# Optimization experiments

Hardware: AMD Instinct MI355X
Metric: run time of the kernel (lower is better)

## Reference

```python
import jax, jax.numpy as jnp
import numpy as np

NUM_ENT = 100000
NUM_REL = 500            # distinct relations; table holds 2*NUM_REL (forward + inverse)
E = 500000               # total edges: first half original, second half reversed
D = 200                  # init_dim = gcn_dim = embed_dim
B = 256
KW, KH = 10, 20          # ConvE reshape: 2*KW*KH == 2*D
NF, KS = 200, 7
FLAT = (2 * KW - KS + 1) * (KH - KS + 1) * NF  # 14*14*200 = 39200
EPS = 1e-5


def setup_inputs() -> dict:
    key = jax.random.key(0)
    k = jax.random.split(key, 24)
    half = E // 2
    src = jax.random.randint(k[0], (half,), 0, NUM_ENT)
    dst = jax.random.randint(k[1], (half,), 0, NUM_ENT)
    et = jax.random.randint(k[2], (half,), 0, NUM_REL)
    edge_index = jnp.stack([jnp.concatenate([src, dst]), jnp.concatenate([dst, src])])
    edge_type = jnp.concatenate([et, et + NUM_REL])
    sub = jax.random.randint(k[3], (B,), 0, NUM_ENT)
    rel = jax.random.randint(k[4], (B,), 0, 2 * NUM_REL)
    g = lambda i, shape, s=0.05: jax.random.normal(k[i], shape, jnp.float32) * s
    return dict(
        sub=sub, rel=rel, edge_index=edge_index, edge_type=edge_type,
        init_embed=g(5, (NUM_ENT, D)), init_rel=g(6, (2 * NUM_REL, D)),
        loop_rel1=g(7, (1, D)), loop_rel2=g(8, (1, D)),
        w_in1=g(9, (D, D)), w_out1=g(10, (D, D)), w_loop1=g(11, (D, D)), w_rel1=g(12, (D, D)), b1=jnp.zeros((D,), jnp.float32),
        w_in2=g(13, (D, D)), w_out2=g(14, (D, D)), w_loop2=g(15, (D, D)), w_rel2=g(16, (D, D)), b2=jnp.zeros((D,), jnp.float32),
        conv_w=g(17, (NF, 1, KS, KS)), conv_b=jnp.zeros((NF,), jnp.float32),
        bn0_g=jnp.ones((1,), jnp.float32), bn0_b=jnp.zeros((1,), jnp.float32),
        bn1_g=jnp.ones((NF,), jnp.float32), bn1_b=jnp.zeros((NF,), jnp.float32),
        bn2_g=jnp.ones((D,), jnp.float32), bn2_b=jnp.zeros((D,), jnp.float32),
        fc_w=g(18, (FLAT, D)), fc_b=jnp.zeros((D,), jnp.float32),
        ent_bias=jnp.zeros((NUM_ENT,), jnp.float32),
    )


def _bn2d(x, g, b):  # eval-mode BN: running mean 0, running var 1
    s = g / jnp.sqrt(1.0 + EPS)
    return x * s[None, :, None, None] + b[None, :, None, None]


def _bn1d(x, g, b):
    return x * (g / jnp.sqrt(1.0 + EPS)) + b


def _agg(x_src, rel_e, dst, w):
    # message = comp(h_src, h_rel) @ W   (subtraction composition), degree-normalized scatter
    m = (x_src - rel_e) @ w                                        # [E/2, D]
    s = jax.ops.segment_sum(m, dst, num_segments=NUM_ENT)          # [N, D]
    deg = jax.ops.segment_sum(jnp.ones(dst.shape, m.dtype), dst, num_segments=NUM_ENT)
    return s / jnp.clip(deg, 1.0)[:, None]


def _ragcn_layer(x, r, ei, et, w_in, w_out, w_loop, w_rel, loop_rel, b):
    half = ei.shape[1] // 2
    src, dst = ei[0], ei[1]
    re = r[et]                                                     # [E, D]
    res = (_agg(x[src[:half]], re[:half], dst[:half], w_in)
           + _agg(x[src[half:]], re[half:], dst[half:], w_out)
           + (x - loop_rel) @ w_loop)
    return jnp.tanh(res / 3.0 + b), r @ w_rel


def _forward(sub, rel, edge_index, edge_type, init_embed, init_rel,
             loop_rel1, loop_rel2, w_in1, w_out1, w_loop1, w_rel1, b1,
             w_in2, w_out2, w_loop2, w_rel2, b2, conv_w, conv_b,
             bn0_g, bn0_b, bn1_g, bn1_b, bn2_g, bn2_b, fc_w, fc_b, ent_bias):
    x, r = _ragcn_layer(init_embed, init_rel, edge_index, edge_type, w_in1, w_out1, w_loop1, w_rel1, loop_rel1, b1)
    x, r = _ragcn_layer(x, r, edge_index, edge_type, w_in2, w_out2, w_loop2, w_rel2, loop_rel2, b2)
    sub_emb = x[sub]                                               # [B, D]
    rel_emb = r[rel]                                               # [B, D]
    # ConvE concat: [B,2,D] -> [B,D,2] -> [B,1,2*KW,KH]
    stk = jnp.transpose(jnp.stack([sub_emb, rel_emb], axis=1), (0, 2, 1)).reshape(-1, 1, 2 * KW, KH)
    h = _bn2d(stk, bn0_g, bn0_b)
    h = jax.lax.conv_general_dilated(h, conv_w, (1, 1), 'VALID',
                                     dimension_numbers=('NCHW', 'OIHW', 'NCHW'))
    h = h + conv_b[None, :, None, None]
    h = jax.nn.relu(_bn2d(h, bn1_g, bn1_b))
    h = h.reshape(-1, FLAT)
    h = h @ fc_w + fc_b
    h = jax.nn.relu(_bn1d(h, bn2_g, bn2_b))
    logits = h @ x.T + ent_bias                                    # [B, NUM_ENT]
    return jax.nn.sigmoid(logits)


def reference(sub, rel, edge_index, edge_type, init_embed, init_rel,
              loop_rel1, loop_rel2, w_in1, w_out1, w_loop1, w_rel1, b1,
              w_in2, w_out2, w_loop2, w_rel2, b2, conv_w, conv_b,
              bn0_g, bn0_b, bn1_g, bn1_b, bn2_g, bn2_b, fc_w, fc_b, ent_bias):
    return _forward(sub, rel, edge_index, edge_type, init_embed, init_rel,
                    loop_rel1, loop_rel2, w_in1, w_out1, w_loop1, w_rel1, b1,
                    w_in2, w_out2, w_loop2, w_rel2, b2, conv_w, conv_b,
                    bn0_g, bn0_b, bn1_g, bn1_b, bn2_g, bn2_b, fc_w, fc_b, ent_bias)
```

## Files before the change

### kernel.cpp

```cpp
#include <hip/hip_runtime.h>
#include <math.h>

#define N_ENT   100000
#define N_REL2  1000
#define E_TOT   500000
#define E_HALF  250000
#define DIM     200
#define BB      256
#define NFILT   200
#define FLATK   39200
#define EPS_BN  1e-5f

#define NROWS   200000
#define SCHUNK  2048
#define SNBLK   ((NROWS + SCHUNK - 1) / SCHUNK)

#define FC_KC   175
#define FC_KLEN 224

typedef __attribute__((ext_vector_type(8))) short bf16x8;
typedef __attribute__((ext_vector_type(4))) float f32x4;

__device__ __forceinline__ unsigned short f2b(float f) {
    union { float f; unsigned u; } c; c.f = f;
    unsigned u = c.u;
    u += 0x7fffu + ((u >> 16) & 1u);
    return (unsigned short)(u >> 16);
}
__device__ __forceinline__ float b2f(unsigned short h) {
    union { unsigned u; float f; } c; c.u = ((unsigned)h) << 16;
    return c.f;
}
__device__ __forceinline__ float fast_tanh(float x) {
    float ax = fabsf(x);
    float e = __expf(-2.0f * ax);
    float t = (1.0f - e) / (1.0f + e);
    return copysignf(t, x);
}

__global__ void convert2_kernel(const float* __restrict__ s1, unsigned short* __restrict__ d1,
                                int n1, const float* __restrict__ s2,
                                unsigned short* __restrict__ d2, int n2, int nb1) {
    int b = blockIdx.x;
    const float* s; unsigned short* d; int n, base;
    if (b < nb1) { s = s1; d = d1; n = n1; base = b; }
    else         { s = s2; d = d2; n = n2; base = b - nb1; }
    int i = (base * 256 + threadIdx.x) * 4;
    if (i + 3 < n) {
        float4 v = *(const float4*)(s + i);
        ushort4 o;
        o.x = f2b(v.x); o.y = f2b(v.y); o.z = f2b(v.z); o.w = f2b(v.w);
        *(ushort4*)(d + i) = o;
    } else {
        for (; i < n; ++i) d[i] = f2b(s[i]);
    }
}

__global__ void wstack_lv_kernel(const float* __restrict__ wIn, const float* __restrict__ wOut,
                                 const float* __restrict__ wLoop,
                                 const float* __restrict__ lr, float* __restrict__ lv,
                                 unsigned short* __restrict__ WTK) {
    if (blockIdx.x == 588) {
        int j = threadIdx.x;
        if (j < DIM) {
            float acc = 0.f;
            for (int k = 0; k < DIM; ++k) acc += lr[k] * wLoop[k * DIM + j];
            lv[j] = acc;
        }
        return;
    }
    int g = blockIdx.x * 256 + threadIdx.x;
    int kk = g & 7;
    int t = g >> 3;
    int col = t % 224;
    int t2 = t / 224;
    int unit = t2 % 28;
    int seg = t2 / 28;
    int k = unit * 8 + kk;
    float v = 0.f;
    if (col < 200 && k < 200)
        v = (seg == 0 ? wIn : seg == 1 ? wOut : wLoop)[k * 200 + col];
    WTK[g] = f2b(v);
}

__global__ void fwt_cwt_kernel(const float* __restrict__ fw, unsigned short* __restrict__ FWT,
                               const float* __restrict__ cw, unsigned short* __restrict__ CWT) {
    __shared__ float t[32][33];
    const int bid = blockIdx.x;
    const int tid = threadIdx.x;
    if (bid >= 8575) {
        int g = (bid - 8575) * 256 + tid;
        int f = g >> 6, k = g & 63;
        CWT[g] = (f < 200 && k < 49) ? f2b(cw[f * 49 + k]) : 0;
        return;
    }
    const int kt = bid % 1225, jt = bid / 1225;
#pragma unroll
    for (int it = 0; it < 4; ++it) {
        int idx = tid + it * 256;
        int kk = idx >> 5, jj = idx & 31;
        int j = jt * 32 + jj;
        t[kk][jj] = (j < 200) ? fw[(size_t)(kt * 32 + kk) * 200 + j] : 0.f;
    }
    __syncthreads();
#pragma unroll
    for (int it = 0; it < 4; ++it) {
        int idx = tid + it * 256;
        int jj = idx >> 5, kk = idx & 31;
        int j = jt * 32 + jj;
        if (j < 208)
            FWT[(size_t)j * FLATK + kt * 32 + kk] = f2b(t[kk][jj]);
    }
}

__global__ void hist_kernel(const int* __restrict__ ei, int* __restrict__ cnt) {
    int e = blockIdx.x * 256 + threadIdx.x;
    if (e >= E_TOT) return;
    int row = ei[E_TOT + e] + (e < E_HALF ? 0 : N_ENT);
    atomicAdd(&cnt[row], 1);
}

__global__ void scan1_kernel(const int* __restrict__ cnt, int* __restrict__ row_start,
                             int* __restrict__ blockSum) {
    __shared__ int tsum[256];
    const int t = threadIdx.x;
    const int base = blockIdx.x * SCHUNK + t * 8;
    int v[8];
    int s = 0;
#pragma unroll
    for (int i = 0; i < 8; ++i) {
        int idx = base + i;
        int c = (idx < NROWS) ? cnt[idx] : 0;
        v[i] = s;
        s += c;
    }
    tsum[t] = s;
    __syncthreads();
    for (int off = 1; off < 256; off <<= 1) {
        int x = (t >= off) ? tsum[t - off] : 0;
        __syncthreads();
        if (t >= off) tsum[t] += x;
        __syncthreads();
    }
    int texc = (t == 0) ? 0 : tsum[t - 1];
    if (t == 0) blockSum[blockIdx.x] = tsum[255];
#pragma unroll
    for (int i = 0; i < 8; ++i) {
        int idx = base + i;
        if (idx < NROWS) row_start[idx] = texc + v[i];
    }
}

__global__ void scan2_kernel(int* __restrict__ blockSum) {
    __shared__ int t[128];
    int i = threadIdx.x;
    int v = (i < SNBLK) ? blockSum[i] : 0;
    t[i] = v;
    __syncthreads();
    for (int off = 1; off < 128; off <<= 1) {
        int x = (i >= off) ? t[i - off] : 0;
        __syncthreads();
        t[i] += x;
        __syncthreads();
    }
    if (i < SNBLK) blockSum[i] = (i == 0) ? 0 : t[i - 1];
}

__global__ void scan3_kernel(int* __restrict__ row_start, int* __restrict__ row_cur,
                             const int* __restrict__ blockSum) {
    int i = blockIdx.x * 256 + threadIdx.x;
    if (i >= NROWS) return;
    int v = row_start[i] + blockSum[i / SCHUNK];
    row_start[i] = v;
    row_cur[i] = v;
}

__global__ void fill_kernel(const int* __restrict__ ei, const int* __restrict__ et,
                            int* __restrict__ row_cur, int2* __restrict__ epair) {
    int e = blockIdx.x * 256 + threadIdx.x;
    if (e >= E_TOT) return;
    int row = ei[E_TOT + e] + (e < E_HALF ? 0 : N_ENT);
    int pos = atomicAdd(&row_cur[row], 1);
    epair[pos] = make_int2(ei[e], et[e]);
}

__global__ void gather_kernel(const unsigned short* __restrict__ x,
                              const unsigned short* __restrict__ r,
                              const int2* __restrict__ epair,
                              const int* __restrict__ row_start, const int* __restrict__ cnt,
                              unsigned short* __restrict__ agg) {
    int wid = blockIdx.x * 4 + (threadIdx.x >> 6);
    if (wid >= NROWS) return;
    int lane = threadIdx.x & 63;
    if (lane >= 50) return;
    int start = row_start[wid];
    int deg = cnt[wid];
    float a0 = 0.f, a1 = 0.f, a2 = 0.f, a3 = 0.f;
    float c0 = 0.f, c1 = 0.f, c2 = 0.f, c3 = 0.f;
    int i = 0;
    for (; i + 2 <= deg; i += 2) {
        int2 e0 = epair[start + i];
        int2 e1 = epair[start + i + 1];
        ushort4 xv0 = *(const ushort4*)(x + (size_t)e0.x * DIM + lane * 4);
        ushort4 rv0 = *(const ushort4*)(r + (size_t)e0.y * DIM + lane * 4);
        ushort4 xv1 = *(const ushort4*)(x + (size_t)e1.x * DIM + lane * 4);
        ushort4 rv1 = *(const ushort4*)(r + (size_t)e1.y * DIM + lane * 4);
        a0 += b2f(xv0.x) - b2f(rv0.x);
        a1 += b2f(xv0.y) - b2f(rv0.y);
        a2 += b2f(xv0.z) - b2f(rv0.z);
        a3 += b2f(xv0.w) - b2f(rv0.w);
        c0 += b2f(xv1.x) - b2f(rv1.x);
        c1 += b2f(xv1.y) - b2f(rv1.y);
        c2 += b2f(xv1.z) - b2f(rv1.z);
        c3 += b2f(xv1.w) - b2f(rv1.w);
    }
    if (i < deg) {
        int2 e = epair[start + i];
        ushort4 xv = *(const ushort4*)(x + (size_t)e.x * DIM + lane * 4);
        ushort4 rv = *(const ushort4*)(r + (size_t)e.y * DIM + lane * 4);
        a0 += b2f(xv.x) - b2f(rv.x);
        a1 += b2f(xv.y) - b2f(rv.y);
        a2 += b2f(xv.z) - b2f(rv.z);
        a3 += b2f(xv.w) - b2f(rv.w);
    }
    float sc = 1.0f / fmaxf((float)deg, 1.0f);
    ushort4 o;
    o.x = f2b((a0 + c0) * sc);
    o.y = f2b((a1 + c1) * sc);
    o.z = f2b((a2 + c2) * sc);
    o.w = f2b((a3 + c3) * sc);
    *(ushort4*)(agg + (size_t)wid * DIM + lane * 4) = o;
}

__global__ void rgemm_kernel(const float* __restrict__ r, const float* __restrict__ w,
                             float* __restrict__ out, unsigned short* __restrict__ outb,
                             int rows) {
    int g = blockIdx.x * 256 + threadIdx.x;
    if (g >= rows * DIM) return;
    int i = g / DIM, j = g - i * DIM;
    float acc = 0.f;
    for (int k = 0; k < DIM; ++k) acc += r[i * DIM + k] * w[k * DIM + j];
    out[g] = acc;
    if (outb) outb[g] = f2b(acc);
}

#define LOAD_A1(g, slot) do {                                                   \
    const unsigned short* Ap_ = Aseg[(g) / 7];                                  \
    apf[slot] = *(const bf16x8*)(Ap_ + (size_t)arow * 200 + ((g) % 7) * 32 + lq * 8); \
} while (0)

#define STAGE_LOAD(s) do {                                                       \
    _Pragma("unroll")                                                            \
    for (int it = 0; it < 4; ++it) {                                             \
        int u = tid + it * 256;                                                  \
        if (u < 896) {                                                           \
            int slot = u / 448;                                                  \
            int rem  = u - slot * 448;                                           \
            int ui   = rem / 112, col = rem - ui * 112;                          \
            int g2   = (s) * 2 + slot;                                           \
            if (g2 < 21) {                                                       \
                int sg = g2 / 7, kc = g2 % 7;                                    \
                vals[it] = *(const int4*)(WTK +                                  \
                    ((size_t)(sg * 28 + kc * 4 + ui) * 224 + colbase + col) * 8);\
            } else vals[it] = make_int4(0, 0, 0, 0);                             \
        }                                                                        \
    }                                                                            \
} while (0)

#define STAGE_WRITE(b) do {                                                      \
    _Pragma("unroll")                                                            \
    for (int it = 0; it < 4; ++it) {                                             \
        int u = tid + it * 256;                                                  \
        if (u < 896) *(int4*)(&Wl[(b)][u * 8]) = vals[it];                       \
    }                                                                            \
} while (0)

__global__ __launch_bounds__(256, 4) void layer_mfma_kernel(
        const unsigned short* __restrict__ aggI, const unsigned short* __restrict__ aggO,
        const unsigned short* __restrict__ xin, const unsigned short* __restrict__ WTK,
        const float* __restrict__ lv, const float* __restrict__ bias,
        unsigned short* __restrict__ out, int nwg) {
    __shared__ unsigned short Wl[2][8 * 112 * 8];
    const int bid = blockIdx.x;
    const int q = nwg >> 3, rr = nwg & 7;
    const int xcd = bid & 7, idx = bid >> 3;
    const int L = (xcd < rr ? xcd * (q + 1) : rr * (q + 1) + (xcd - rr) * q) + idx;
    const int rowblk  = L >> 1;
    const int colbase = (L & 1) * 112;

    const int tid  = threadIdx.x;
    const int wm   = tid >> 6;
    const int lane = tid & 63;
    const int lr   = lane & 15;
    const int lq   = lane >> 4;
    const int row0 = rowblk * 64;
    const int arow = row0 + wm * 16 + lr;

    const unsigned short* const Aseg[3] = { aggI, aggO, xin };

    f32x4 acc[7];
#pragma unroll
    for (int n = 0; n < 7; ++n) acc[n] = (f32x4){0.f, 0.f, 0.f, 0.f};

    bf16x8 apf[4];
    LOAD_A1(0, 0);
    LOAD_A1(1, 1);
    LOAD_A1(2, 2);

    int4 vals[4];

    STAGE_LOAD(0);
    STAGE_WRITE(0);
    __syncthreads();

#pragma unroll
    for (int p = 0; p < 11; ++p) {
        if (p < 10) STAGE_LOAD(p + 1);
        const int NC = (p < 10) ? 2 : 1;
#pragma unroll
        for (int cc = 0; cc < NC; ++cc) {
            const int g = p * 2 + cc;
            if (g + 3 < 21) LOAD_A1(g + 3, (g + 3) & 3);
            __builtin_amdgcn_s_setprio(1);
#pragma unroll
            for (int n = 0; n < 7; ++n) {
                bf16x8 b = *(const bf16x8*)(&Wl[p & 1][((cc * 4 + lq) * 112 + n * 16 + lr) * 8]);
                acc[n] = __builtin_amdgcn_mfma_f32_16x16x32_bf16(apf[g & 3], b, acc[n], 0, 0, 0);
            }
            __builtin_amdgcn_s_setprio(0);
        }
        if (p < 10) STAGE_WRITE((p + 1) & 1);
        __syncthreads();
    }

    {
        int rbase = row0 + wm * 16 + lq * 4;
#pragma unroll
        for (int n = 0; n < 7; ++n) {
            int col = colbase + n * 16 + lr;
            if (col < 200) {
                float lvc = lv[col], bc = bias[col];
#pragma unroll
                for (int r2 = 0; r2 < 4; ++r2) {
                    int row = rbase + r2;
                    if (row < N_ENT) {
                        float v = (acc[n][r2] - lvc) * (1.0f / 3.0f) + bc;
                        out[(size_t)row * 200 + col] = f2b(fast_tanh(v));
                    }
                }
            }
        }
    }
}

__global__ void img_kernel(const unsigned short* __restrict__ x, const float* __restrict__ r,
                           const int* __restrict__ sub, const int* __restrict__ rel,
                           const float* __restrict__ bn0g, const float* __restrict__ bn0b,
                           unsigned short* __restrict__ img) {
    int g = blockIdx.x * 256 + threadIdx.x;
    if (g >= BB * 2 * DIM) return;
    int b = g / 400, l = g - b * 400;
    int d = l >> 1;
    float v = (l & 1) ? r[(size_t)rel[b] * DIM + d] : b2f(x[(size_t)sub[b] * DIM + d]);
    float s0 = bn0g[0] * rsqrtf(1.0f + EPS_BN);
    img[g] = f2b(v * s0 + bn0b[0]);
}

__global__ void im2col_kernel(const unsigned short* __restrict__ img,
                              unsigned short* __restrict__ IM) {
    int g = blockIdx.x * 256 + threadIdx.x;
    if (g >= 50176 * 64) return;
    int row = g >> 6, k = g & 63;
    int b = row / 196, p = row - b * 196;
    int h = p / 14, w = p - h * 14;
    unsigned short v = 0;
    if (k < 49) {
        int i = k / 7, j = k - i * 7;
        v = img[b * 400 + (h + i) * 20 + (w + j)];
    }
    IM[g] = v;
}

__global__ __launch_bounds__(256) void conv_mfma_kernel(
        const unsigned short* __restrict__ IM, const unsigned short* __restrict__ CWT,
        const float* __restrict__ cb, const float* __restrict__ bn1g,
        const float* __restrict__ bn1b, unsigned short* __restrict__ CO_B) {
    const int tid  = threadIdx.x;
    const int row0 = blockIdx.x * 128;
    const int wave = tid >> 6;
    const int lane = tid & 63;
    const int lr   = lane & 15;
    const int lq   = lane >> 4;
    const int arow = row0 + wave * 32 + lr;

    f32x4 acc[2][13];
#pragma unroll
    for (int m = 0; m < 2; ++m)
#pragma unroll
        for (int n = 0; n < 13; ++n) acc[m][n] = (f32x4){0.f, 0.f, 0.f, 0.f};

#pragma unroll
    for (int c = 0; c < 2; ++c) {
        const int k = c * 32 + lq * 8;
        bf16x8 a0 = *(const bf16x8*)(IM + (size_t)arow * 64 + k);
        bf16x8 a1 = *(const bf16x8*)(IM + (size_t)(arow + 16) * 64 + k);
#pragma unroll
        for (int n = 0; n < 13; ++n) {
            bf16x8 b = *(const bf16x8*)(CWT + (size_t)(n * 16 + lr) * 64 + k);
            acc[0][n] = __builtin_amdgcn_mfma_f32_16x16x32_bf16(a0, b, acc[0][n], 0, 0, 0);
            acc[1][n] = __builtin_amdgcn_mfma_f32_16x16x32_bf16(a1, b, acc[1][n], 0, 0, 0);
        }
    }

#pragma unroll
    for (int m = 0; m < 2; ++m) {
        int grow_base = row0 + wave * 32 + m * 16 + lq * 4;
#pragma unroll
        for (int n = 0; n < 13; ++n) {
            int col = n * 16 + lr;
            if (col < 200) {
                float s1 = bn1g[col] * rsqrtf(1.0f + EPS_BN);
                float t1 = bn1b[col];
                float cbf = cb[col];
#pragma unroll
                for (int r = 0; r < 4; ++r) {
                    int grow = grow_base + r;
                    int b = grow / 196, p = grow - b * 196;
                    float v = fmaxf((acc[m][n][r] + cbf) * s1 + t1, 0.f);
                    CO_B[(size_t)b * FLATK + col * 196 + p] = f2b(v);
                }
            }
        }
    }
}

__global__ __launch_bounds__(256) void fc_mfma_kernel(
        const unsigned short* __restrict__ CO_B, const unsigned short* __restrict__ FWT,
        float* __restrict__ partials) {
    const int tid  = threadIdx.x;
    const int kc   = blockIdx.x >> 2;
    const int mb   = blockIdx.x & 3;
    const int wave = tid >> 6;
    const int lane = tid & 63;
    const int lr   = lane & 15;
    const int lq   = lane >> 4;
    const int m0   = mb * 64 + wave * 16;

    f32x4 acc[13];
#pragma unroll
    for (int n = 0; n < 13; ++n) acc[n] = (f32x4){0.f, 0.f, 0.f, 0.f};

#pragma unroll
    for (int s = 0; s < 7; ++s) {
        const int k = kc * FC_KLEN + s * 32 + lq * 8;
        bf16x8 a = *(const bf16x8*)(CO_B + (size_t)(m0 + lr) * FLATK + k);
#pragma unroll
        for (int n = 0; n < 13; ++n) {
            bf16x8 b = *(const bf16x8*)(FWT + (size_t)(n * 16 + lr) * FLATK + k);
            acc[n] = __builtin_amdgcn_mfma_f32_16x16x32_bf16(a, b, acc[n], 0, 0, 0);
        }
    }

    float* slab = partials + (size_t)kc * (BB * 208);
#pragma unroll
    for (int n = 0; n < 13; ++n) {
        int col = n * 16 + lr;
#pragma unroll
        for (int r = 0; r < 4; ++r) {
            int row = m0 + lq * 4 + r;
            slab[(size_t)row * 208 + col] = acc[n][r];
        }
    }
}

__global__ void fc_reduce_kernel(const float* __restrict__ partials,
                                 const float* __restrict__ fcb,
                                 const float* __restrict__ g2, const float* __restrict__ b2v,
                                 unsigned short* __restrict__ hb) {
    int g = blockIdx.x * 256 + threadIdx.x;
    if (g >= BB * 224) return;
    int b = g / 224, j = g - b * 224;
    unsigned short o = 0;
    if (j < 200) {
        float s = 0.f;
        const float* p = partials + (size_t)b * 208 + j;
#pragma unroll 5
        for (int c = 0; c < FC_KC; ++c)
            s += p[(size_t)c * (BB * 208)];
        float v = (s + fcb[j]) * (g2[j] * rsqrtf(1.0f + EPS_BN)) + b2v[j];
        o = f2b(fmaxf(v, 0.f));
    }
    hb[g] = o;
}

#define LOAD_HB(g, buf) do {                                                    \
    const unsigned short* base_ = hb + (size_t)brow * 224 + (g) * 32 + lq * 8;  \
    buf[0] = *(const bf16x8*)(base_);                                           \
    buf[1] = *(const bf16x8*)(base_ + 16 * 224);                                \
} while (0)

__global__ __launch_bounds__(512, 2) void logits_mfma_kernel(
        const unsigned short* __restrict__ x, const unsigned short* __restrict__ hb,
        const float* __restrict__ eb, float* __restrict__ out, int nwg) {
    __shared__ unsigned short Xl[112 * 136];
    const int bid = blockIdx.x;
    const int q = nwg >> 3, rr = nwg & 7;
    const int xcd = bid & 7, idx = bid >> 3;
    const int nb = (xcd < rr ? xcd * (q + 1) : rr * (q + 1) + (xcd - rr) * q) + idx;
    const int ent0 = nb * 112;

    const int tid  = threadIdx.x;
    const int wave = tid >> 6;
    const int mh   = wave >> 2;
    const int wm   = wave & 3;
    const int lane = tid & 63;
    const int lr   = lane & 15;
    const int lq   = lane >> 4;
    const int brow = mh * 128 + wm * 32 + lr;

    f32x4 acc[2][7];
#pragma unroll
    for (int m = 0; m < 2; ++m)
#pragma unroll
        for (int n = 0; n < 7; ++n) acc[m][n] = (f32x4){0.f, 0.f, 0.f, 0.f};

    bf16x8 apf[3][2];
    LOAD_HB(0, apf[0]);
    LOAD_HB(1, apf[1]);

#pragma unroll
    for (int ph = 0; ph < 2; ++ph) {
        if (ph) __syncthreads();
        if (ph == 0) {
#pragma unroll
            for (int it = 0; it < 4; ++it) {
                int u = tid + it * 512;
                if (u < 1792) {
                    int row = u >> 4, c = u & 15;
                    int ent = ent0 + row;
                    int4 v = make_int4(0, 0, 0, 0);
                    if (ent < N_ENT)
                        v = *(const int4*)(x + (size_t)ent * 200 + c * 8);
                    *(int4*)(&Xl[row * 136 + c * 8]) = v;
                }
            }
        } else {
            for (int u = tid; u < 1344; u += 512) {
                int row = u / 12, c = u - row * 12;
                int gu = 16 + c;
                int ent = ent0 + row;
                int4 v = make_int4(0, 0, 0, 0);
                if (ent < N_ENT && gu < 25)
                    v = *(const int4*)(x + (size_t)ent * 200 + gu * 8);
                *(int4*)(&Xl[row * 136 + c * 8]) = v;
            }
        }
        __syncthreads();
        const int NC = (ph == 0) ? 4 : 3;
#pragma unroll
        for (int cc = 0; cc < NC; ++cc) {
            const int g = (ph ? 4 : 0) + cc;
            if (g + 2 < 7) LOAD_HB(g + 2, apf[(g + 2) % 3]);
#pragma unroll
            for (int n = 0; n < 7; ++n) {
                bf16x8 b = *(const bf16x8*)(&Xl[(n * 16 + lr) * 136 + cc * 32 + lq * 8]);
                acc[0][n] = __builtin_amdgcn_mfma_f32_16x16x32_bf16(apf[g % 3][0], b, acc[0][n], 0, 0, 0);
                acc[1][n] = __builtin_amdgcn_mfma_f32_16x16x32_bf16(apf[g % 3][1], b, acc[1][n], 0, 0, 0);
            }
        }
    }

#pragma unroll
    for (int m = 0; m < 2; ++m) {
        int b_base = mh * 128 + wm * 32 + m * 16 + lq * 4;
#pragma unroll
        for (int n = 0; n < 7; ++n) {
            int ent = ent0 + n * 16 + lr;
            if (ent < N_ENT) {
                float bias = eb[ent];
#pragma unroll
                for (int r = 0; r < 4; ++r) {
                    float v = acc[m][n][r] + bias;
                    out[(size_t)(b_base + r) * N_ENT + ent] = 1.0f / (1.0f + __expf(-v));
                }
            }
        }
    }
}

extern "C" void kernel_launch(void* const* d_in, const int* in_sizes, int n_in,
                              void* d_out, int out_size, void* d_ws, size_t ws_size,
                              hipStream_t stream) {
    const int*   sub        = (const int*)  d_in[0];
    const int*   rel        = (const int*)  d_in[1];
    const int*   edge_index = (const int*)  d_in[2];
    const int*   edge_type  = (const int*)  d_in[3];
    const float* init_embed = (const float*)d_in[4];
    const float* init_rel   = (const float*)d_in[5];
    const float* loop_rel1  = (const float*)d_in[6];
    const float* loop_rel2  = (const float*)d_in[7];
    const float* w_in1      = (const float*)d_in[8];
    const float* w_out1     = (const float*)d_in[9];
    const float* w_loop1    = (const float*)d_in[10];
    const float* w_rel1     = (const float*)d_in[11];
    const float* b1         = (const float*)d_in[12];
    const float* w_in2      = (const float*)d_in[13];
    const float* w_out2     = (const float*)d_in[14];
    const float* w_loop2    = (const float*)d_in[15];
    const float* w_rel2     = (const float*)d_in[16];
    const float* b2         = (const float*)d_in[17];
    const float* conv_w     = (const float*)d_in[18];
    const float* conv_b     = (const float*)d_in[19];
    const float* bn0_g      = (const float*)d_in[20];
    const float* bn0_b      = (const float*)d_in[21];
    const float* bn1_g      = (const float*)d_in[22];
    const float* bn1_b      = (const float*)d_in[23];
    const float* bn2_g      = (const float*)d_in[24];
    const float* bn2_b      = (const float*)d_in[25];
    const float* fc_w       = (const float*)d_in[26];
    const float* fc_b       = (const float*)d_in[27];
    const float* ent_bias   = (const float*)d_in[28];

    unsigned short* aggb = (unsigned short*)d_ws;
    unsigned short* x0b  = aggb + 40000000;
    unsigned short* x1b  = x0b  + 20000000;
    unsigned short* r0b  = x1b  + 20000000;
    unsigned short* r1b  = r0b  + 200000;
    unsigned short* WTK  = r1b  + 200000;
    unsigned short* img  = WTK  + 150528;
    unsigned short* IM   = img  + 102400;
    unsigned short* CWT  = IM   + 3211264;
    unsigned short* CO_B = CWT  + 13312;
    unsigned short* hb16 = CO_B + 10035200;
    unsigned short* FWT  = hb16 + 57344;
    float* fbase = (float*)(FWT + 8153600);
    float* r1f      = fbase;
    float* r2f      = r1f  + 200000;
    float* lv       = r2f  + 200000;
    float* partials = lv   + 256;

    int2* epair    = (int2*)CO_B;
    int* cnt       = (int*)(epair + E_TOT);
    int* row_start = cnt  + NROWS;
    int* row_cur   = row_start + NROWS;
    int* blockSum  = row_cur + NROWS;

    unsigned short* aggIb = aggb;
    unsigned short* aggOb = aggb + (size_t)N_ENT * DIM;
    unsigned short* x2b   = x0b;

    const int gather_blocks = (NROWS + 3) / 4;
    const int layer_nwg     = ((N_ENT + 63) / 64) * 2;
    const int logits_nwg    = (N_ENT + 111) / 112;
    const int cvt_nb1       = (N_ENT * DIM / 4 + 255) / 256;
    const int cvt_nb2       = (N_REL2 * DIM / 4 + 255) / 256;

    convert2_kernel<<<cvt_nb1 + cvt_nb2, 256, 0, stream>>>(init_embed, x0b, N_ENT * DIM,
                                                           init_rel, r0b, N_REL2 * DIM, cvt_nb1);
    hipMemsetAsync(cnt, 0, (size_t)NROWS * 4, stream);
    hist_kernel<<<(E_TOT + 255) / 256, 256, 0, stream>>>(edge_index, cnt);
    scan1_kernel<<<SNBLK, 256, 0, stream>>>(cnt, row_start, blockSum);
    scan2_kernel<<<1, 128, 0, stream>>>(blockSum);
    scan3_kernel<<<(NROWS + 255) / 256, 256, 0, stream>>>(row_start, row_cur, blockSum);
    fill_kernel<<<(E_TOT + 255) / 256, 256, 0, stream>>>(edge_index, edge_type, row_cur, epair);

    wstack_lv_kernel<<<589, 256, 0, stream>>>(w_in1, w_out1, w_loop1, loop_rel1, lv, WTK);
    gather_kernel<<<gather_blocks, 256, 0, stream>>>(x0b, r0b, epair, row_start, cnt, aggb);
    layer_mfma_kernel<<<layer_nwg, 256, 0, stream>>>(aggIb, aggOb, x0b, WTK, lv, b1, x1b, layer_nwg);
    rgemm_kernel<<<(N_REL2 * DIM + 255) / 256, 256, 0, stream>>>(init_rel, w_rel1, r1f, r1b, N_REL2);

    wstack_lv_kernel<<<589, 256, 0, stream>>>(w_in2, w_out2, w_loop2, loop_rel2, lv, WTK);
    gather_kernel<<<gather_blocks, 256, 0, stream>>>(x1b, r1b, epair, row_start, cnt, aggb);
    layer_mfma_kernel<<<layer_nwg, 256, 0, stream>>>(aggIb, aggOb, x1b, WTK, lv, b2, x2b, layer_nwg);
    rgemm_kernel<<<(N_REL2 * DIM + 255) / 256, 256, 0, stream>>>(r1f, w_rel2, r2f,
                                                                 (unsigned short*)nullptr, N_REL2);

    img_kernel<<<(BB * 400 + 255) / 256, 256, 0, stream>>>(x2b, r2f, sub, rel,
                                                           bn0_g, bn0_b, img);
    im2col_kernel<<<(50176 * 64 + 255) / 256, 256, 0, stream>>>(img, IM);
    fwt_cwt_kernel<<<8575 + 52, 256, 0, stream>>>(fc_w, FWT, conv_w, CWT);
    conv_mfma_kernel<<<50176 / 128, 256, 0, stream>>>(IM, CWT, conv_b, bn1_g, bn1_b, CO_B);
    fc_mfma_kernel<<<FC_KC * 4, 256, 0, stream>>>(CO_B, FWT, partials);
    fc_reduce_kernel<<<(BB * 224 + 255) / 256, 256, 0, stream>>>(partials, fc_b, bn2_g, bn2_b, hb16);

    logits_mfma_kernel<<<logits_nwg, 512, 0, stream>>>(x2b, hb16, ent_bias, (float*)d_out,
                                                       logits_nwg);
}
```

Measured before the change: 557.3 us.

## Stream layer weights directly into LDS and fuse image build into im2col

The layer GEMM now stages weight tiles with direct global-to-LDS loads instead of going through registers and then a separate LDS write. This frees registers and drops the extra write step. Separately, the img kernel is merged into im2col, so each im2col element reads the embeddings directly and applies the BN0 scaling, which removes one launch and one intermediate buffer. The direct LDS loads rely on the asynchronous load being ordered before the existing barrier, and the fused im2col repeats the gather and scaling for each of the 49 taps.

```diff
diff --git a/kernel.cpp b/kernel.cpp
--- a/kernel.cpp
+++ b/kernel.cpp
@@ -20,6 +20,9 @@
 
 typedef __attribute__((ext_vector_type(8))) short bf16x8;
 typedef __attribute__((ext_vector_type(4))) float f32x4;
+
+#define GLOBAL_AS __attribute__((address_space(1)))
+#define LDS_AS    __attribute__((address_space(3)))
 
 __device__ __forceinline__ unsigned short f2b(float f) {
     union { float f; unsigned u; } c; c.f = f;
@@ -249,29 +252,22 @@
     apf[slot] = *(const bf16x8*)(Ap_ + (size_t)arow * 200 + ((g) % 7) * 32 + lq * 8); \
 } while (0)
 
-#define STAGE_LOAD(s) do {                                                       \
+#define STAGE_GLD(s, b) do {                                                     \
     _Pragma("unroll")                                                            \
     for (int it = 0; it < 4; ++it) {                                             \
         int u = tid + it * 256;                                                  \
-        if (u < 896) {                                                           \
-            int slot = u / 448;                                                  \
-            int rem  = u - slot * 448;                                           \
-            int ui   = rem / 112, col = rem - ui * 112;                          \
-            int g2   = (s) * 2 + slot;                                           \
-            if (g2 < 21) {                                                       \
-                int sg = g2 / 7, kc = g2 % 7;                                    \
-                vals[it] = *(const int4*)(WTK +                                  \
-                    ((size_t)(sg * 28 + kc * 4 + ui) * 224 + colbase + col) * 8);\
-            } else vals[it] = make_int4(0, 0, 0, 0);                             \
+        int slot = u / 448;                                                      \
+        int rem  = u - slot * 448;                                               \
+        int ui   = rem / 112, col = rem - ui * 112;                              \
+        int g2   = (s) * 2 + slot;                                               \
+        if (u < 896 && g2 < 21) {                                                \
+            int sg = g2 / 7, kc = g2 % 7;                                        \
+            const unsigned short* gp = WTK +                                     \
+                ((size_t)(sg * 28 + kc * 4 + ui) * 224 + colbase + col) * 8;     \
+            __builtin_amdgcn_global_load_lds(                                    \
+                (const GLOBAL_AS unsigned int*)(const void*)gp,                  \
+                (LDS_AS unsigned int*)(void*)(&Wl[(b)][u * 8]), 16, 0, 0);       \
         }                                                                        \
-    }                                                                            \
-} while (0)
-
-#define STAGE_WRITE(b) do {                                                      \
-    _Pragma("unroll")                                                            \
-    for (int it = 0; it < 4; ++it) {                                             \
-        int u = tid + it * 256;                                                  \
-        if (u < 896) *(int4*)(&Wl[(b)][u * 8]) = vals[it];                       \
     }                                                                            \
 } while (0)
 
@@ -307,15 +303,12 @@
     LOAD_A1(1, 1);
     LOAD_A1(2, 2);
 
-    int4 vals[4];
-
-    STAGE_LOAD(0);
-    STAGE_WRITE(0);
+    STAGE_GLD(0, 0);
     __syncthreads();
 
 #pragma unroll
     for (int p = 0; p < 11; ++p) {
-        if (p < 10) STAGE_LOAD(p + 1);
+        if (p < 10) STAGE_GLD(p + 1, (p + 1) & 1);
         const int NC = (p < 10) ? 2 : 1;
 #pragma unroll
         for (int cc = 0; cc < NC; ++cc) {
@@ -329,7 +322,6 @@
             }
             __builtin_amdgcn_s_setprio(0);
         }
-        if (p < 10) STAGE_WRITE((p + 1) & 1);
         __syncthreads();
     }
 
@@ -353,32 +345,25 @@
     }
 }
 
-__global__ void img_kernel(const unsigned short* __restrict__ x, const float* __restrict__ r,
-                           const int* __restrict__ sub, const int* __restrict__ rel,
-                           const float* __restrict__ bn0g, const float* __restrict__ bn0b,
-                           unsigned short* __restrict__ img) {
-    int g = blockIdx.x * 256 + threadIdx.x;
-    if (g >= BB * 2 * DIM) return;
-    int b = g / 400, l = g - b * 400;
-    int d = l >> 1;
-    float v = (l & 1) ? r[(size_t)rel[b] * DIM + d] : b2f(x[(size_t)sub[b] * DIM + d]);
-    float s0 = bn0g[0] * rsqrtf(1.0f + EPS_BN);
-    img[g] = f2b(v * s0 + bn0b[0]);
-}
-
-__global__ void im2col_kernel(const unsigned short* __restrict__ img,
+__global__ void im2col_kernel(const unsigned short* __restrict__ x, const float* __restrict__ r,
+                              const int* __restrict__ sub, const int* __restrict__ rel,
+                              const float* __restrict__ bn0g, const float* __restrict__ bn0b,
                               unsigned short* __restrict__ IM) {
     int g = blockIdx.x * 256 + threadIdx.x;
     if (g >= 50176 * 64) return;
     int row = g >> 6, k = g & 63;
     int b = row / 196, p = row - b * 196;
     int h = p / 14, w = p - h * 14;
-    unsigned short v = 0;
+    unsigned short o = 0;
     if (k < 49) {
         int i = k / 7, j = k - i * 7;
-        v = img[b * 400 + (h + i) * 20 + (w + j)];
-    }
-    IM[g] = v;
+        int l = (h + i) * 20 + (w + j);
+        int d = l >> 1;
+        float v = (l & 1) ? r[(size_t)rel[b] * DIM + d] : b2f(x[(size_t)sub[b] * DIM + d]);
+        float s0 = bn0g[0] * rsqrtf(1.0f + EPS_BN);
+        o = f2b(v * s0 + bn0b[0]);
+    }
+    IM[g] = o;
 }
 
 __global__ __launch_bounds__(256) void conv_mfma_kernel(
@@ -675,9 +660,8 @@
     rgemm_kernel<<<(N_REL2 * DIM + 255) / 256, 256, 0, stream>>>(r1f, w_rel2, r2f,
                                                                  (unsigned short*)nullptr, N_REL2);
 
-    img_kernel<<<(BB * 400 + 255) / 256, 256, 0, stream>>>(x2b, r2f, sub, rel,
-                                                           bn0_g, bn0_b, img);
-    im2col_kernel<<<(50176 * 64 + 255) / 256, 256, 0, stream>>>(img, IM);
+    im2col_kernel<<<(50176 * 64 + 255) / 256, 256, 0, stream>>>(x2b, r2f, sub, rel,
+                                                                bn0_g, bn0_b, IM);
     fwt_cwt_kernel<<<8575 + 52, 256, 0, stream>>>(fc_w, FWT, conv_w, CWT);
     conv_mfma_kernel<<<50176 / 128, 256, 0, stream>>>(IM, CWT, conv_b, bn1_g, bn1_b, CO_B);
     fc_mfma_kernel<<<FC_KC * 4, 256, 0, stream>>>(CO_B, FWT, partials);
```

New measurement: 560.1 us. About the same (+0.5%).
